# Performance work log

Hardware: AMD Instinct MI355X
Metric: run time of the kernel (lower is better)

Reference implementation:

```python
import jax, jax.numpy as jnp
import numpy as np

N_NODES = 50000
N_EDGES = 800000
D_IN = 128
D_HID = 128
N_CLS = 40


def setup_inputs() -> dict:
    key = jax.random.key(0)
    ks = jax.random.split(key, 8)
    x = jax.random.normal(ks[0], (N_NODES, D_IN), dtype=jnp.float32)
    edge_index = jax.random.randint(ks[1], (2, N_EDGES), 0, N_NODES, dtype=jnp.int32)
    s1 = 1.0 / np.sqrt(D_IN)
    s2 = 1.0 / np.sqrt(D_HID)
    W1 = jax.random.normal(ks[2], (D_IN, D_HID), dtype=jnp.float32) * s1
    b1 = jnp.zeros((D_HID,), dtype=jnp.float32)
    W2 = jax.random.normal(ks[3], (D_HID, D_HID), dtype=jnp.float32) * s2
    b2 = jnp.zeros((D_HID,), dtype=jnp.float32)
    Wc = jax.random.normal(ks[4], (D_HID, N_CLS), dtype=jnp.float32) * s2
    bc = jnp.zeros((N_CLS,), dtype=jnp.float32)
    return {"x": x, "edge_index": edge_index, "W1": W1, "b1": b1,
            "W2": W2, "b2": b2, "Wc": Wc, "bc": bc, "conv_time": 30}


def _gcn_graph(edge_index, n, dtype):
    # add self-loops, compute symmetric GCN normalization D^-1/2 A D^-1/2
    loops = jnp.arange(n, dtype=edge_index.dtype)
    src = jnp.concatenate([edge_index[0], loops])
    dst = jnp.concatenate([edge_index[1], loops])
    deg = jax.ops.segment_sum(jnp.ones_like(src, dtype=dtype), dst, num_segments=n)
    dinv = jnp.where(deg > 0, jax.lax.rsqrt(jnp.maximum(deg, 1.0)), 0.0).astype(dtype)
    w = dinv[src] * dinv[dst]  # [E+N] edge weights
    return src, dst, w


def _propagate_k(h, src, dst, w, n, k):
    # apply normalized aggregation k times (k is a static Python int-compatible value)
    def body(_, hh):
        return jax.ops.segment_sum(hh[src] * w[:, None], dst, num_segments=n)
    return jax.lax.fori_loop(0, k, body, h)


def reference(x, edge_index, W1, b1, W2, b2, Wc, bc, conv_time):
    n = x.shape[0]
    src, dst, w = _gcn_graph(edge_index, n, x.dtype)
    # conv1: linear only (conv_time=0), relu; dropout is identity in eval mode
    h = jax.nn.relu(x @ W1 + b1)
    # conv2: linear + conv_time propagation hops, relu
    h = jax.nn.relu(_propagate_k(h @ W2 + b2, src, dst, w, n, conv_time))
    # cls: linear + 1 propagation hop
    out = _propagate_k(h @ Wc + bc, src, dst, w, n, 1)
    return out
```

## Files before the change

### kernel.cpp

```cpp
#include <hip/hip_runtime.h>
#include <hip/hip_bf16.h>

#define NN 50000
#define NE 800000
#define DH 128
#define NCLS 40
#define HOPS 30

typedef unsigned int uint32;
typedef unsigned short ushort16;
typedef __attribute__((ext_vector_type(8))) short short8v;
typedef __attribute__((ext_vector_type(4))) float float4v;


__device__ __forceinline__ ushort16 bfbits(float x) {
    __hip_bfloat16 b = __float2bfloat16(x);
    return *reinterpret_cast<ushort16*>(&b);
}

__device__ __forceinline__ float bflo(uint32 u) { return __uint_as_float(u << 16); }
__device__ __forceinline__ float bfhi(uint32 u) { return __uint_as_float(u & 0xffff0000u); }

__device__ __forceinline__ uint32 pack2(float a, float b) {
    return (uint32)bfbits(a) | ((uint32)bfbits(b) << 16);
}


__global__ void count_deg(const int* __restrict__ dst, int* __restrict__ cnt) {
    int e = blockIdx.x * blockDim.x + threadIdx.x;
    if (e < NE) atomicAdd(&cnt[dst[e]], 1);
}

__global__ void calc_dinv(const int* __restrict__ cnt, float* __restrict__ dinv) {
    int v = blockIdx.x * blockDim.x + threadIdx.x;
    if (v < NN) dinv[v] = rsqrtf((float)cnt[v] + 1.0f);
}

__global__ void scan1(const int* __restrict__ cnt, int* __restrict__ rowptr,
                      int* __restrict__ bsum) {
    __shared__ int s[1024];
    int t = threadIdx.x;
    int i = blockIdx.x * 1024 + t;
    int v = (i < NN) ? cnt[i] : 0;
    s[t] = v;
    __syncthreads();
    for (int off = 1; off < 1024; off <<= 1) {
        int add = (t >= off) ? s[t - off] : 0;
        __syncthreads();
        s[t] += add;
        __syncthreads();
    }
    if (i < NN) rowptr[i] = s[t] - v;
    if (t == 1023) bsum[blockIdx.x] = s[1023];
}

__global__ void scan2(int* __restrict__ bsum, int* __restrict__ rowptr, int nb) {
    if (blockIdx.x == 0 && threadIdx.x == 0) {
        int run = 0;
        for (int b = 0; b < nb; ++b) { int v = bsum[b]; bsum[b] = run; run += v; }
        rowptr[NN] = run;
    }
}

__global__ void scan3(int* __restrict__ rowptr, const int* __restrict__ bsum,
                      int* __restrict__ cursor) {
    int i = blockIdx.x * 1024 + threadIdx.x;
    if (i < NN) {
        int r = rowptr[i] + bsum[blockIdx.x];
        rowptr[i] = r;
        cursor[i] = r;
    }
}

__global__ void fill_csr(const int* __restrict__ src, const int* __restrict__ dst,
                         const float* __restrict__ dinv, int* __restrict__ cursor,
                         int2* __restrict__ csr) {
    int e = blockIdx.x * blockDim.x + threadIdx.x;
    if (e < NE) {
        int s = src[e], d = dst[e];
        int p = atomicAdd(&cursor[d], 1);
        csr[p] = make_int2(s, __float_as_int(dinv[s] * dinv[d]));
    }
}


__global__ void prep_wt(const float* __restrict__ W1, const float* __restrict__ W2,
                        ushort16* __restrict__ w1t, ushort16* __restrict__ w2t) {
    int i = blockIdx.x * 256 + threadIdx.x;
    if (i < 16384) {
        int n = i >> 7, k = i & 127;
        w1t[n * 128 + k] = bfbits(W1[k * 128 + n]);
    } else {
        int j = i - 16384;
        int n = j >> 7, k = j & 127;
        w2t[n * 128 + k] = bfbits(W2[k * 128 + n]);
    }
}

__global__ void prep_wc(const float* __restrict__ Wc, ushort16* __restrict__ wct) {
    int i = blockIdx.x * 256 + threadIdx.x;
    if (i < 48 * 128) {
        int n = i >> 7, k = i & 127;
        wct[i] = (n < NCLS) ? bfbits(Wc[k * NCLS + n]) : (ushort16)0;
    }
}


template <bool AF32, bool RELU>
__global__ __launch_bounds__(256) void conv_mfma(const void* __restrict__ Ap,
                                                 const ushort16* __restrict__ WT,
                                                 const float* __restrict__ bias,
                                                 ushort16* __restrict__ C) {
    const int t = threadIdx.x;
    const int w = t >> 6;
    const int l = t & 63;
    const int rb = blockIdx.x * 128 + w * 32;
    const int lr = l & 15;
    const int lk = (l >> 4) * 8;

    short8v afr[2][4];
#pragma unroll
    for (int rt = 0; rt < 2; ++rt) {
        int row = rb + rt * 16 + lr;
        if (row > NN - 1) row = NN - 1;
#pragma unroll
        for (int ks = 0; ks < 4; ++ks) {
            int k0 = ks * 32 + lk;
            if (AF32) {
                const float* ap = (const float*)Ap + (size_t)row * 128 + k0;
                float4 f0 = *(const float4*)ap;
                float4 f1 = *(const float4*)(ap + 4);
                short8v s;
                s[0] = (short)bfbits(f0.x); s[1] = (short)bfbits(f0.y);
                s[2] = (short)bfbits(f0.z); s[3] = (short)bfbits(f0.w);
                s[4] = (short)bfbits(f1.x); s[5] = (short)bfbits(f1.y);
                s[6] = (short)bfbits(f1.z); s[7] = (short)bfbits(f1.w);
                afr[rt][ks] = s;
            } else {
                afr[rt][ks] = *(const short8v*)((const ushort16*)Ap +
                                                (size_t)row * 128 + k0);
            }
        }
    }

    float4v acc[2][8];
#pragma unroll
    for (int rt = 0; rt < 2; ++rt)
#pragma unroll
        for (int ct = 0; ct < 8; ++ct)
            acc[rt][ct] = (float4v){0.f, 0.f, 0.f, 0.f};

#pragma unroll
    for (int ks = 0; ks < 4; ++ks) {
        short8v bfr[8];
#pragma unroll
        for (int ct = 0; ct < 8; ++ct)
            bfr[ct] = *(const short8v*)(WT + (size_t)(ct * 16 + lr) * 128 +
                                        ks * 32 + lk);
#pragma unroll
        for (int ct = 0; ct < 8; ++ct) {
            acc[0][ct] = __builtin_amdgcn_mfma_f32_16x16x32_bf16(
                afr[0][ks], bfr[ct], acc[0][ct], 0, 0, 0);
            acc[1][ct] = __builtin_amdgcn_mfma_f32_16x16x32_bf16(
                afr[1][ks], bfr[ct], acc[1][ct], 0, 0, 0);
        }
    }

#pragma unroll
    for (int ct = 0; ct < 8; ++ct) {
        int col = ct * 16 + lr;
        float bv = bias[col];
#pragma unroll
        for (int rt = 0; rt < 2; ++rt) {
#pragma unroll
            for (int r = 0; r < 4; ++r) {
                int row = rb + rt * 16 + (l >> 4) * 4 + r;
                if (row < NN) {
                    float o = acc[rt][ct][r] + bv;
                    if (RELU) o = fmaxf(o, 0.f);
                    C[(size_t)row * 128 + col] = bfbits(o);
                }
            }
        }
    }
}


__global__ __launch_bounds__(256) void cls_mfma(const ushort16* __restrict__ q,
                                                const ushort16* __restrict__ WcT,
                                                const float* __restrict__ bc,
                                                const float* __restrict__ psum,
                                                float* __restrict__ out) {
    const int t = threadIdx.x;
    const int w = t >> 6;
    const int l = t & 63;
    const int rb = blockIdx.x * 128 + w * 32;
    const int lr = l & 15;
    const int lk = (l >> 4) * 8;

    short8v afr[2][4];
#pragma unroll
    for (int rt = 0; rt < 2; ++rt) {
        int row = rb + rt * 16 + lr;
        if (row > NN - 1) row = NN - 1;
#pragma unroll
        for (int ks = 0; ks < 4; ++ks)
            afr[rt][ks] = *(const short8v*)(q + (size_t)row * 128 + ks * 32 + lk);
    }

    float4v acc[2][3];
#pragma unroll
    for (int rt = 0; rt < 2; ++rt)
#pragma unroll
        for (int ct = 0; ct < 3; ++ct)
            acc[rt][ct] = (float4v){0.f, 0.f, 0.f, 0.f};

#pragma unroll
    for (int ks = 0; ks < 4; ++ks) {
        short8v bfr[3];
#pragma unroll
        for (int ct = 0; ct < 3; ++ct)
            bfr[ct] = *(const short8v*)(WcT + (size_t)(ct * 16 + lr) * 128 +
                                        ks * 32 + lk);
#pragma unroll
        for (int ct = 0; ct < 3; ++ct) {
            acc[0][ct] = __builtin_amdgcn_mfma_f32_16x16x32_bf16(
                afr[0][ks], bfr[ct], acc[0][ct], 0, 0, 0);
            acc[1][ct] = __builtin_amdgcn_mfma_f32_16x16x32_bf16(
                afr[1][ks], bfr[ct], acc[1][ct], 0, 0, 0);
        }
    }

#pragma unroll
    for (int rt = 0; rt < 2; ++rt) {
#pragma unroll
        for (int r = 0; r < 4; ++r) {
            int row = rb + rt * 16 + (l >> 4) * 4 + r;
            if (row < NN) {
                float pv = psum[row];
#pragma unroll
                for (int ct = 0; ct < 3; ++ct) {
                    int col = ct * 16 + lr;
                    if (col < NCLS)
                        out[(size_t)row * NCLS + col] =
                            acc[rt][ct][r] + pv * bc[col];
                }
            }
        }
    }
}


__global__ __launch_bounds__(256) void prop_row(const uint32* __restrict__ hin,
                                                uint32* __restrict__ hout,
                                                const int* __restrict__ rowptr,
                                                const int2* __restrict__ csr,
                                                const float* __restrict__ dinv,
                                                float* __restrict__ psum,
                                                int relu, int wpsum) {
    const int v = blockIdx.x * 4 + (threadIdx.x >> 6);
    const int l = threadIdx.x & 63;
    if (v >= NN) return;

    const float dv = dinv[v];
    const float wself = dv * dv;
    float accp = wself;

    float a0, a1;
    {
        uint32 u = hin[(size_t)v * 64 + l];
        a0 = wself * bflo(u);
        a1 = wself * bfhi(u);
    }

    int e = rowptr[v];
    const int end = rowptr[v + 1];
    for (; e + 4 <= end; e += 4) {
        int2 c0 = csr[e];
        int2 c1 = csr[e + 1];
        int2 c2 = csr[e + 2];
        int2 c3 = csr[e + 3];
        uint32 g0 = hin[(size_t)c0.x * 64 + l];
        uint32 g1 = hin[(size_t)c1.x * 64 + l];
        uint32 g2 = hin[(size_t)c2.x * 64 + l];
        uint32 g3 = hin[(size_t)c3.x * 64 + l];
        float w0 = __int_as_float(c0.y);
        float w1 = __int_as_float(c1.y);
        float w2 = __int_as_float(c2.y);
        float w3 = __int_as_float(c3.y);
        accp += (w0 + w1) + (w2 + w3);
        a0 += w0 * bflo(g0) + w1 * bflo(g1) + w2 * bflo(g2) + w3 * bflo(g3);
        a1 += w0 * bfhi(g0) + w1 * bfhi(g1) + w2 * bfhi(g2) + w3 * bfhi(g3);
    }
    for (; e < end; ++e) {
        int2 c0 = csr[e];
        uint32 g0 = hin[(size_t)c0.x * 64 + l];
        float w0 = __int_as_float(c0.y);
        accp += w0;
        a0 += w0 * bflo(g0);
        a1 += w0 * bfhi(g0);
    }

    if (relu) { a0 = fmaxf(a0, 0.f); a1 = fmaxf(a1, 0.f); }

    hout[(size_t)v * 64 + l] = pack2(a0, a1);
    if (wpsum && l == 0) psum[v] = accp;
}


extern "C" void kernel_launch(void* const* d_in, const int* in_sizes, int n_in,
                              void* d_out, int out_size, void* d_ws, size_t ws_size,
                              hipStream_t stream) {
    const float* x   = (const float*)d_in[0];
    const int* edge  = (const int*)d_in[1];
    const float* W1  = (const float*)d_in[2];
    const float* b1  = (const float*)d_in[3];
    const float* W2  = (const float*)d_in[4];
    const float* b2  = (const float*)d_in[5];
    const float* Wc  = (const float*)d_in[6];
    const float* bc  = (const float*)d_in[7];
    const int* esrc = edge;
    const int* edst = edge + NE;
    float* out = (float*)d_out;

    char* w = (char*)d_ws;
    auto alloc = [&](size_t bytes) { void* p = (void*)w; w += (bytes + 255) & ~(size_t)255; return p; };
    int*      cnt     = (int*)     alloc((size_t)NN * 4);
    float*    dinv    = (float*)   alloc((size_t)NN * 4);
    int*      rowptr  = (int*)     alloc((size_t)(NN + 1) * 4);
    int*      bsum    = (int*)     alloc(64 * 4);
    int*      cursor  = (int*)     alloc((size_t)NN * 4);
    int2*     csr     = (int2*)    alloc((size_t)NE * 8);
    ushort16* w1t     = (ushort16*)alloc(128 * 128 * 2);
    ushort16* w2t     = (ushort16*)alloc(128 * 128 * 2);
    ushort16* wct     = (ushort16*)alloc(48 * 128 * 2);
    ushort16* h0b     = (ushort16*)alloc((size_t)NN * DH * 2);
    uint32*   hb0     = (uint32*)  alloc((size_t)NN * DH * 2);
    uint32*   hb1     = (uint32*)  alloc((size_t)NN * DH * 2);
    float*    psum    = (float*)   alloc((size_t)NN * 4);

    const int NB_SCAN = (NN + 1023) / 1024;
    const int NCHUNK = (NN + 127) / 128;

    hipMemsetAsync(cnt, 0, (size_t)NN * 4, stream);
    count_deg<<<(NE + 255) / 256, 256, 0, stream>>>(edst, cnt);
    calc_dinv<<<(NN + 255) / 256, 256, 0, stream>>>(cnt, dinv);
    scan1<<<NB_SCAN, 1024, 0, stream>>>(cnt, rowptr, bsum);
    scan2<<<1, 64, 0, stream>>>(bsum, rowptr, NB_SCAN);
    scan3<<<NB_SCAN, 1024, 0, stream>>>(rowptr, bsum, cursor);
    fill_csr<<<(NE + 255) / 256, 256, 0, stream>>>(esrc, edst, dinv, cursor, csr);
    prep_wt<<<128, 256, 0, stream>>>(W1, W2, w1t, w2t);
    prep_wc<<<24, 256, 0, stream>>>(Wc, wct);

    conv_mfma<true, true><<<NCHUNK, 256, 0, stream>>>(x, w1t, b1, h0b);
    conv_mfma<false, false><<<NCHUNK, 256, 0, stream>>>(h0b, w2t, b2,
                                                        (ushort16*)hb0);

    uint32* cur = hb0;
    uint32* alt = hb1;
    for (int hop = 0; hop < HOPS; ++hop) {
        prop_row<<<(NN + 3) / 4, 256, 0, stream>>>(cur, alt, rowptr, csr, dinv,
                                                   psum, (hop == HOPS - 1) ? 1 : 0, 0);
        uint32* tmp = cur; cur = alt; alt = tmp;
    }
    prop_row<<<(NN + 3) / 4, 256, 0, stream>>>(cur, (uint32*)h0b, rowptr, csr, dinv,
                                               psum, 0, 1);

    cls_mfma<<<NCHUNK, 256, 0, stream>>>(h0b, wct, bc, psum, out);
}
```

Baseline: 1.414 ms.

## Use 16-lane groups with 16-byte gathers and degree-sorted node order for propagation

The propagation kernel now assigns 16 lanes per node instead of a full 64-lane wavefront, and each lane loads a uint4 holding 8 bf16 features. Every wave therefore handles four nodes and issues wider gathers. Nodes are also processed in an order sorted by in-degree, built with a histogram and scatter permutation, so the four nodes in a wave have similar edge counts and less divergence. The cost is three small setup kernels, an extra indirection through perm, and output writes that are no longer in node order.

After: 1.486 ms. 1.05x slower.

```diff
diff --git a/kernel.cpp b/kernel.cpp
--- a/kernel.cpp
+++ b/kernel.cpp
@@ -18,8 +18,16 @@
     return *reinterpret_cast<ushort16*>(&b);
 }
 
-__device__ __forceinline__ float bflo(uint32 u) { return __uint_as_float(u << 16); }
-__device__ __forceinline__ float bfhi(uint32 u) { return __uint_as_float(u & 0xffff0000u); }
+__device__ __forceinline__ void unpack8(uint4 u, float* f) {
+    f[0] = __uint_as_float(u.x << 16);
+    f[1] = __uint_as_float(u.x & 0xffff0000u);
+    f[2] = __uint_as_float(u.y << 16);
+    f[3] = __uint_as_float(u.y & 0xffff0000u);
+    f[4] = __uint_as_float(u.z << 16);
+    f[5] = __uint_as_float(u.z & 0xffff0000u);
+    f[6] = __uint_as_float(u.w << 16);
+    f[7] = __uint_as_float(u.w & 0xffff0000u);
+}
 
 __device__ __forceinline__ uint32 pack2(float a, float b) {
     return (uint32)bfbits(a) | ((uint32)bfbits(b) << 16);
@@ -80,6 +88,28 @@
         int s = src[e], d = dst[e];
         int p = atomicAdd(&cursor[d], 1);
         csr[p] = make_int2(s, __float_as_int(dinv[s] * dinv[d]));
+    }
+}
+
+
+__global__ void hist_deg(const int* __restrict__ cnt, int* __restrict__ hist) {
+    int v = blockIdx.x * blockDim.x + threadIdx.x;
+    if (v < NN) atomicAdd(&hist[min(cnt[v], 63)], 1);
+}
+
+__global__ void scan_hist(const int* __restrict__ hist, int* __restrict__ bcur) {
+    if (blockIdx.x == 0 && threadIdx.x == 0) {
+        int run = 0;
+        for (int i = 0; i < 64; ++i) { bcur[i] = run; run += hist[i]; }
+    }
+}
+
+__global__ void scatter_perm(const int* __restrict__ cnt, int* __restrict__ bcur,
+                             int* __restrict__ perm) {
+    int v = blockIdx.x * blockDim.x + threadIdx.x;
+    if (v < NN) {
+        int p = atomicAdd(&bcur[min(cnt[v], 63)], 1);
+        perm[p] = v;
     }
 }
 
@@ -251,26 +281,29 @@
 }
 
 
-__global__ __launch_bounds__(256) void prop_row(const uint32* __restrict__ hin,
-                                                uint32* __restrict__ hout,
+__global__ __launch_bounds__(256) void prop_g16(const uint4* __restrict__ hin,
+                                                uint4* __restrict__ hout,
                                                 const int* __restrict__ rowptr,
                                                 const int2* __restrict__ csr,
                                                 const float* __restrict__ dinv,
+                                                const int* __restrict__ perm,
                                                 float* __restrict__ psum,
                                                 int relu, int wpsum) {
-    const int v = blockIdx.x * 4 + (threadIdx.x >> 6);
-    const int l = threadIdx.x & 63;
-    if (v >= NN) return;
+    const int gi = blockIdx.x * 16 + (threadIdx.x >> 4);
+    const int l = threadIdx.x & 15;
+    if (gi >= NN) return;
+    const int v = perm[gi];
 
     const float dv = dinv[v];
     const float wself = dv * dv;
     float accp = wself;
 
-    float a0, a1;
+    float acc[8];
     {
-        uint32 u = hin[(size_t)v * 64 + l];
-        a0 = wself * bflo(u);
-        a1 = wself * bfhi(u);
+        float f[8];
+        unpack8(hin[(size_t)v * 16 + l], f);
+#pragma unroll
+        for (int j = 0; j < 8; ++j) acc[j] = wself * f[j];
     }
 
     int e = rowptr[v];
@@ -280,30 +313,46 @@
         int2 c1 = csr[e + 1];
         int2 c2 = csr[e + 2];
         int2 c3 = csr[e + 3];
-        uint32 g0 = hin[(size_t)c0.x * 64 + l];
-        uint32 g1 = hin[(size_t)c1.x * 64 + l];
-        uint32 g2 = hin[(size_t)c2.x * 64 + l];
-        uint32 g3 = hin[(size_t)c3.x * 64 + l];
+        uint4 u0 = hin[(size_t)c0.x * 16 + l];
+        uint4 u1 = hin[(size_t)c1.x * 16 + l];
+        uint4 u2 = hin[(size_t)c2.x * 16 + l];
+        uint4 u3 = hin[(size_t)c3.x * 16 + l];
         float w0 = __int_as_float(c0.y);
         float w1 = __int_as_float(c1.y);
         float w2 = __int_as_float(c2.y);
         float w3 = __int_as_float(c3.y);
         accp += (w0 + w1) + (w2 + w3);
-        a0 += w0 * bflo(g0) + w1 * bflo(g1) + w2 * bflo(g2) + w3 * bflo(g3);
-        a1 += w0 * bfhi(g0) + w1 * bfhi(g1) + w2 * bfhi(g2) + w3 * bfhi(g3);
+        float f0[8], f1[8], f2[8], f3[8];
+        unpack8(u0, f0);
+        unpack8(u1, f1);
+        unpack8(u2, f2);
+        unpack8(u3, f3);
+#pragma unroll
+        for (int j = 0; j < 8; ++j)
+            acc[j] += (w0 * f0[j] + w1 * f1[j]) + (w2 * f2[j] + w3 * f3[j]);
     }
     for (; e < end; ++e) {
         int2 c0 = csr[e];
-        uint32 g0 = hin[(size_t)c0.x * 64 + l];
+        uint4 u0 = hin[(size_t)c0.x * 16 + l];
         float w0 = __int_as_float(c0.y);
         accp += w0;
-        a0 += w0 * bflo(g0);
-        a1 += w0 * bfhi(g0);
-    }
-
-    if (relu) { a0 = fmaxf(a0, 0.f); a1 = fmaxf(a1, 0.f); }
-
-    hout[(size_t)v * 64 + l] = pack2(a0, a1);
+        float f0[8];
+        unpack8(u0, f0);
+#pragma unroll
+        for (int j = 0; j < 8; ++j) acc[j] += w0 * f0[j];
+    }
+
+    if (relu) {
+#pragma unroll
+        for (int j = 0; j < 8; ++j) acc[j] = fmaxf(acc[j], 0.f);
+    }
+
+    uint4 u;
+    u.x = pack2(acc[0], acc[1]);
+    u.y = pack2(acc[2], acc[3]);
+    u.z = pack2(acc[4], acc[5]);
+    u.w = pack2(acc[6], acc[7]);
+    hout[(size_t)v * 16 + l] = u;
     if (wpsum && l == 0) psum[v] = accp;
 }
 
@@ -331,24 +380,31 @@
     int*      bsum    = (int*)     alloc(64 * 4);
     int*      cursor  = (int*)     alloc((size_t)NN * 4);
     int2*     csr     = (int2*)    alloc((size_t)NE * 8);
+    int*      hist    = (int*)     alloc(64 * 4);
+    int*      bcur    = (int*)     alloc(64 * 4);
+    int*      perm    = (int*)     alloc((size_t)NN * 4);
     ushort16* w1t     = (ushort16*)alloc(128 * 128 * 2);
     ushort16* w2t     = (ushort16*)alloc(128 * 128 * 2);
     ushort16* wct     = (ushort16*)alloc(48 * 128 * 2);
     ushort16* h0b     = (ushort16*)alloc((size_t)NN * DH * 2);
-    uint32*   hb0     = (uint32*)  alloc((size_t)NN * DH * 2);
-    uint32*   hb1     = (uint32*)  alloc((size_t)NN * DH * 2);
+    uint4*    hb0     = (uint4*)   alloc((size_t)NN * DH * 2);
+    uint4*    hb1     = (uint4*)   alloc((size_t)NN * DH * 2);
     float*    psum    = (float*)   alloc((size_t)NN * 4);
 
     const int NB_SCAN = (NN + 1023) / 1024;
     const int NCHUNK = (NN + 127) / 128;
 
     hipMemsetAsync(cnt, 0, (size_t)NN * 4, stream);
+    hipMemsetAsync(hist, 0, 64 * 4, stream);
     count_deg<<<(NE + 255) / 256, 256, 0, stream>>>(edst, cnt);
     calc_dinv<<<(NN + 255) / 256, 256, 0, stream>>>(cnt, dinv);
     scan1<<<NB_SCAN, 1024, 0, stream>>>(cnt, rowptr, bsum);
     scan2<<<1, 64, 0, stream>>>(bsum, rowptr, NB_SCAN);
     scan3<<<NB_SCAN, 1024, 0, stream>>>(rowptr, bsum, cursor);
     fill_csr<<<(NE + 255) / 256, 256, 0, stream>>>(esrc, edst, dinv, cursor, csr);
+    hist_deg<<<(NN + 255) / 256, 256, 0, stream>>>(cnt, hist);
+    scan_hist<<<1, 64, 0, stream>>>(hist, bcur);
+    scatter_perm<<<(NN + 255) / 256, 256, 0, stream>>>(cnt, bcur, perm);
     prep_wt<<<128, 256, 0, stream>>>(W1, W2, w1t, w2t);
     prep_wc<<<24, 256, 0, stream>>>(Wc, wct);
 
@@ -356,15 +412,16 @@
     conv_mfma<false, false><<<NCHUNK, 256, 0, stream>>>(h0b, w2t, b2,
                                                         (ushort16*)hb0);
 
-    uint32* cur = hb0;
-    uint32* alt = hb1;
+    uint4* cur = hb0;
+    uint4* alt = hb1;
     for (int hop = 0; hop < HOPS; ++hop) {
-        prop_row<<<(NN + 3) / 4, 256, 0, stream>>>(cur, alt, rowptr, csr, dinv,
-                                                   psum, (hop == HOPS - 1) ? 1 : 0, 0);
-        uint32* tmp = cur; cur = alt; alt = tmp;
-    }
-    prop_row<<<(NN + 3) / 4, 256, 0, stream>>>(cur, (uint32*)h0b, rowptr, csr, dinv,
-                                               psum, 0, 1);
+        prop_g16<<<(NN + 15) / 16, 256, 0, stream>>>(cur, alt, rowptr, csr, dinv,
+                                                     perm, psum,
+                                                     (hop == HOPS - 1) ? 1 : 0, 0);
+        uint4* tmp = cur; cur = alt; alt = tmp;
+    }
+    prop_g16<<<(NN + 15) / 16, 256, 0, stream>>>(cur, (uint4*)h0b, rowptr, csr,
+                                                 dinv, perm, psum, 0, 1);
 
     cls_mfma<<<NCHUNK, 256, 0, stream>>>(h0b, wct, bc, psum, out);
 }
```
